# Performance work log

Measured on AMD Instinct MI355X. Metric: run time of the kernel, lower is better.

Reference implementation:

```python
import jax, jax.numpy as jnp
import numpy as np

B, S, D_IN, D_H, D_OUT = 32, 512, 512, 1024, 512


def setup_inputs() -> dict:
    key = jax.random.key(0)
    ks = jax.random.split(key, 12)
    sc_g = 1.0 / np.sqrt(D_IN + D_H)
    sc_fc = 1.0 / np.sqrt(D_H)
    return {
        "x": jax.random.normal(ks[0], (B, S, D_IN), jnp.float32),
        "W_f": jax.random.normal(ks[1], (D_IN + D_H, D_H), jnp.float32) * sc_g,
        "b_f": jax.random.normal(ks[2], (D_H,), jnp.float32) * sc_g,
        "W_i": jax.random.normal(ks[3], (D_IN + D_H, D_H), jnp.float32) * sc_g,
        "b_i": jax.random.normal(ks[4], (D_H,), jnp.float32) * sc_g,
        "W_g": jax.random.normal(ks[5], (D_IN + D_H, D_H), jnp.float32) * sc_g,
        "b_g": jax.random.normal(ks[6], (D_H,), jnp.float32) * sc_g,
        "W_o": jax.random.normal(ks[7], (D_IN + D_H, D_H), jnp.float32) * sc_g,
        "b_o": jax.random.normal(ks[8], (D_H,), jnp.float32) * sc_g,
        "W_fc": jax.random.normal(ks[9], (D_H, D_OUT), jnp.float32) * sc_fc,
        "b_fc": jax.random.normal(ks[10], (D_OUT,), jnp.float32) * sc_fc,
    }


def _lstm(x, W_f, b_f, W_i, b_i, W_g, b_g, W_o, b_o, W_fc, b_fc):
    b, s, _ = x.shape
    h0 = jnp.zeros((b, W_f.shape[1]), x.dtype)
    c0 = jnp.zeros_like(h0)

    def step(carry, x_t):
        h, c = carry
        comb = jnp.concatenate([x_t, h], axis=1)  # [B, D_in+D_h]
        f = jax.nn.sigmoid(comb @ W_f + b_f)
        i = jax.nn.sigmoid(comb @ W_i + b_i)
        g = jnp.tanh(comb @ W_g + b_g)
        o = jax.nn.sigmoid(comb @ W_o + b_o)
        c = f * c + i * g
        h = o * jnp.tanh(c)
        return (h, c), h

    _, hs = jax.lax.scan(step, (h0, c0), jnp.swapaxes(x, 0, 1))  # [S, B, D_h]
    hs = jnp.swapaxes(hs, 0, 1)  # [B, S, D_h]
    return hs @ W_fc + b_fc  # [B, S, D_out]


def reference(x, W_f, b_f, W_i, b_i, W_g, b_g, W_o, b_o, W_fc, b_fc):
    return _lstm(x, W_f, b_f, W_i, b_i, W_g, b_g, W_o, b_o, W_fc, b_fc)
```

## Files before the change

### kernel.cpp

```cpp
#include <hip/hip_runtime.h>

typedef short short8 __attribute__((ext_vector_type(8)));
typedef float f32x4 __attribute__((ext_vector_type(4)));
typedef unsigned short u16;

#define Bz   32
#define Sz   512
#define DIN  512
#define DH   1024
#define DOUT 512
#define KTOT 1536
#define NWG  256
#define NTH  256
#define TPW  12

__device__ __forceinline__ u16 bf_rne(float f) {
  unsigned b = __float_as_uint(f);
  return (u16)((b + 0x7fffu + ((b >> 16) & 1u)) >> 16);
}
__device__ __forceinline__ float bf_f(u16 h) { return __uint_as_float(((unsigned)h) << 16); }
__device__ __forceinline__ void bf_split(float f, u16& hi, u16& lo) {
  hi = bf_rne(f);
  lo = bf_rne(f - bf_f(hi));
}

__device__ __forceinline__ float sigm(float v) { return 1.0f / (1.0f + __expf(-v)); }

__device__ __forceinline__ f32x4 mfma16(short8 a, short8 b, f32x4 c) {
  return __builtin_amdgcn_mfma_f32_16x16x32_bf16(a, b, c, 0, 0, 0);
}

__device__ __forceinline__ void grid_bar(unsigned* __restrict__ arrive,
                                         unsigned* __restrict__ rel,
                                         int wg, int tid, unsigned round) {
  __syncthreads();
  if (wg == 0) {
    if (tid > 0) {
      while (__hip_atomic_load(&arrive[tid * 32], __ATOMIC_RELAXED,
                               __HIP_MEMORY_SCOPE_AGENT) < round)
        __builtin_amdgcn_s_sleep(1);
    }
    __builtin_amdgcn_fence(__ATOMIC_ACQUIRE, "agent");
    __syncthreads();
    if (tid == 0)
      __hip_atomic_store(rel, round, __ATOMIC_RELEASE, __HIP_MEMORY_SCOPE_AGENT);
  } else {
    if (tid == 0) {
      __hip_atomic_store(&arrive[wg * 32], round, __ATOMIC_RELEASE,
                         __HIP_MEMORY_SCOPE_AGENT);
      while (__hip_atomic_load(rel, __ATOMIC_RELAXED,
                               __HIP_MEMORY_SCOPE_AGENT) < round)
        __builtin_amdgcn_s_sleep(1);
      __builtin_amdgcn_fence(__ATOMIC_ACQUIRE, "agent");
    }
    __syncthreads();
  }
}

__global__ __launch_bounds__(256)
void xsplit(const float* __restrict__ x, u16* __restrict__ xhi, u16* __restrict__ xlo) {
  const int i = (blockIdx.x * 256 + threadIdx.x) * 4;
  const float4 v = *(const float4*)(x + i);
  u16 h0, l0, h1, l1, h2, l2, h3, l3;
  bf_split(v.x, h0, l0); bf_split(v.y, h1, l1);
  bf_split(v.z, h2, l2); bf_split(v.w, h3, l3);
  ushort4 hv = {h0, h1, h2, h3}, lv = {l0, l1, l2, l3};
  *(ushort4*)(xhi + i) = hv;
  *(ushort4*)(xlo + i) = lv;
}

__global__ __launch_bounds__(NTH, 1)
void lstm_rec(const u16* __restrict__ xhi, const u16* __restrict__ xlo,
              const float* __restrict__ Wf, const float* __restrict__ bfv,
              const float* __restrict__ Wi, const float* __restrict__ biv,
              const float* __restrict__ Wg, const float* __restrict__ bgv,
              const float* __restrict__ Wo, const float* __restrict__ bov,
              u16* __restrict__ hhi, u16* __restrict__ hlo,
              float* __restrict__ hs,
              unsigned* __restrict__ arrive, unsigned* __restrict__ rel)
{
  __shared__ __align__(16) float pdump[4][2][64][4];
  __shared__ float csh[Bz][4];
  __shared__ float bsh[16];

  const int tid  = threadIdx.x;
  const int wg   = blockIdx.x;
  const int wid  = tid >> 6;
  const int lane = tid & 63;
  const int c    = lane & 15;
  const int q    = lane >> 4;
  const int g    = c & 3;
  const int jl   = c >> 2;
  const int col  = wg * 4 + jl;

  const float* Wsrc = (g == 0) ? Wf : (g == 1) ? Wi : (g == 2) ? Wg : Wo;
  short8 Bhi[TPW], Blo[TPW];
  #pragma unroll
  for (int tt = 0; tt < TPW; ++tt) {
    const int k0 = (wid * TPW + tt) * 32 + q * 8;
    short8 bh, bl;
    #pragma unroll
    for (int i = 0; i < 8; ++i) {
      u16 h, l;
      bf_split(Wsrc[(k0 + i) * DH + col], h, l);
      bh[i] = (short)h; bl[i] = (short)l;
    }
    Bhi[tt] = bh; Blo[tt] = bl;
  }
  if (tid < 16) {
    const int g2 = tid & 3;
    const float* bsrc = (g2 == 0) ? bfv : (g2 == 1) ? biv : (g2 == 2) ? bgv : bov;
    bsh[tid] = bsrc[wg * 4 + (tid >> 2)];
  }
  if (tid < 128) {
    csh[tid & 31][tid >> 5] = 0.0f;
    const int idx = wg * 128 + tid;
    hhi[idx] = 0; hlo[idx] = 0;
  }
  grid_bar(arrive, rel, wg, tid, 1u);

  const int bA = lane & 15;

  for (int t = 0; t < Sz; ++t) {
    const u16* __restrict__ hh = hhi + (t & 1) * (Bz * DH);
    const u16* __restrict__ hl = hlo + (t & 1) * (Bz * DH);

    f32x4 a_hh0 = {0.f,0.f,0.f,0.f}, a_hl0 = a_hh0, a_lh0 = a_hh0;
    f32x4 a_hh1 = a_hh0, a_hl1 = a_hh0, a_lh1 = a_hh0;

    #pragma unroll
    for (int tt = 0; tt < TPW; ++tt) {
      const int k = (wid * TPW + tt) * 32 + q * 8;
      short8 Ah0, Al0, Ah1, Al1;
      if (k < DIN) {
        Ah0 = *(const short8*)(xhi + ((bA * Sz + t) * DIN + k));
        Ah1 = *(const short8*)(xhi + (((bA + 16) * Sz + t) * DIN + k));
        Al0 = *(const short8*)(xlo + ((bA * Sz + t) * DIN + k));
        Al1 = *(const short8*)(xlo + (((bA + 16) * Sz + t) * DIN + k));
      } else {
        const int kh = k - DIN;
        Ah0 = *(const short8*)(hh + bA * DH + kh);
        Ah1 = *(const short8*)(hh + (bA + 16) * DH + kh);
        Al0 = *(const short8*)(hl + bA * DH + kh);
        Al1 = *(const short8*)(hl + (bA + 16) * DH + kh);
      }
      a_hh0 = mfma16(Ah0, Bhi[tt], a_hh0);
      a_hl0 = mfma16(Ah0, Blo[tt], a_hl0);
      a_lh0 = mfma16(Al0, Bhi[tt], a_lh0);
      a_hh1 = mfma16(Ah1, Bhi[tt], a_hh1);
      a_hl1 = mfma16(Ah1, Blo[tt], a_hl1);
      a_lh1 = mfma16(Al1, Bhi[tt], a_lh1);
    }
    const f32x4 acc0 = a_hh0 + a_hl0 + a_lh0;
    const f32x4 acc1 = a_hh1 + a_hl1 + a_lh1;
    *(f32x4*)&pdump[wid][0][lane][0] = acc0;
    *(f32x4*)&pdump[wid][1][lane][0] = acc1;
    __syncthreads();

    if (tid < 128) {
      const int b = tid & 31, j = tid >> 5;
      const int m = b >> 4, r = b & 15, rg = r & 3;
      float G[4];
      #pragma unroll
      for (int g2 = 0; g2 < 4; ++g2) {
        const int ln = (r >> 2) * 16 + (j * 4 + g2);
        G[g2] = bsh[j * 4 + g2] + pdump[0][m][ln][rg] + pdump[1][m][ln][rg]
              + pdump[2][m][ln][rg] + pdump[3][m][ln][rg];
      }
      const float fv = sigm(G[0]);
      const float iv = sigm(G[1]);
      const float gv = tanhf(G[2]);
      const float ov = sigm(G[3]);
      const float cn = fv * csh[b][j] + iv * gv;
      csh[b][j] = cn;
      const float hv = ov * tanhf(cn);
      u16 hx, lx; bf_split(hv, hx, lx);
      const int par = ((t + 1) & 1) * (Bz * DH);
      hhi[par + b * DH + wg * 4 + j] = hx;
      hlo[par + b * DH + wg * 4 + j] = lx;
      hs[(b * Sz + t) * DH + wg * 4 + j] = hv;
    }
    grid_bar(arrive, rel, wg, tid, (unsigned)(t + 2));
  }
}

__global__ __launch_bounds__(256)
void lstm_fc(const float* __restrict__ hs, const float* __restrict__ Wfc,
             const float* __restrict__ bfc, float* __restrict__ out)
{
  __shared__ __align__(16) float Ash[16][68];
  __shared__ __align__(16) float Bsh[16][68];
  const int tid = threadIdx.x;
  const int mt = (int)(blockIdx.x >> 3) * 64;
  const int nt = (int)(blockIdx.x & 7) * 64;
  const int ty = tid >> 4, tx = tid & 15;
  const int am = tid & 63, ak = (tid >> 6) * 4;
  const int bk = tid >> 4, bn = (tid & 15) * 4;
  float acc[4][4] = {};
  for (int k0 = 0; k0 < DH; k0 += 16) {
    const float4 av = *(const float4*)&hs[(mt + am) * DH + k0 + ak];
    const float4 bv = *(const float4*)&Wfc[(k0 + bk) * DOUT + nt + bn];
    Ash[ak + 0][am] = av.x;
    Ash[ak + 1][am] = av.y;
    Ash[ak + 2][am] = av.z;
    Ash[ak + 3][am] = av.w;
    *(float4*)&Bsh[bk][bn] = bv;
    __syncthreads();
    #pragma unroll
    for (int kk = 0; kk < 16; ++kk) {
      const float4 a = *(const float4*)&Ash[kk][ty * 4];
      const float4 b = *(const float4*)&Bsh[kk][tx * 4];
      const float avv[4] = {a.x, a.y, a.z, a.w};
      const float bvv[4] = {b.x, b.y, b.z, b.w};
      #pragma unroll
      for (int i = 0; i < 4; ++i)
        #pragma unroll
        for (int j = 0; j < 4; ++j)
          acc[i][j] = fmaf(avv[i], bvv[j], acc[i][j]);
    }
    __syncthreads();
  }
  const float4 bb = *(const float4*)&bfc[nt + tx * 4];
  const float bias[4] = {bb.x, bb.y, bb.z, bb.w};
  #pragma unroll
  for (int i = 0; i < 4; ++i) {
    float4 o;
    o.x = acc[i][0] + bias[0];
    o.y = acc[i][1] + bias[1];
    o.z = acc[i][2] + bias[2];
    o.w = acc[i][3] + bias[3];
    *(float4*)&out[(mt + ty * 4 + i) * DOUT + nt + tx * 4] = o;
  }
}

extern "C" void kernel_launch(void* const* d_in, const int* in_sizes, int n_in,
                              void* d_out, int out_size, void* d_ws, size_t ws_size,
                              hipStream_t stream) {
  const float* x   = (const float*)d_in[0];
  const float* Wf  = (const float*)d_in[1];
  const float* bf  = (const float*)d_in[2];
  const float* Wi  = (const float*)d_in[3];
  const float* bi  = (const float*)d_in[4];
  const float* Wg  = (const float*)d_in[5];
  const float* bg  = (const float*)d_in[6];
  const float* Wo  = (const float*)d_in[7];
  const float* bo  = (const float*)d_in[8];
  const float* Wfc = (const float*)d_in[9];
  const float* bfc = (const float*)d_in[10];
  float* out = (float*)d_out;

  char* w = (char*)d_ws;
  unsigned* arrive = (unsigned*)w;
  unsigned* rel    = (unsigned*)(w + 32768);
  size_t off = 65536;
  u16* hhi = (u16*)(w + off);                         off += 2u * Bz * DH * sizeof(u16);
  u16* hlo = (u16*)(w + off);                         off += 2u * Bz * DH * sizeof(u16);
  u16* xhi = (u16*)(w + off);                         off += (size_t)Bz * Sz * DIN * sizeof(u16);
  u16* xlo = (u16*)(w + off);                         off += (size_t)Bz * Sz * DIN * sizeof(u16);
  float* hs = (float*)(w + off);

  hipMemsetAsync(d_ws, 0, 65536, stream);

  const int xN = Bz * Sz * DIN;
  hipLaunchKernelGGL(xsplit, dim3(xN / (256 * 4)), dim3(256), 0, stream, x, xhi, xlo);

  hipLaunchKernelGGL(lstm_rec, dim3(NWG), dim3(NTH), 0, stream,
                     xhi, xlo, Wf, bf, Wi, bi, Wg, bg, Wo, bo, hhi, hlo, hs,
                     arrive, rel);

  hipLaunchKernelGGL(lstm_fc, dim3((Bz * Sz / 64) * (DOUT / 64)), dim3(256), 0, stream,
                     hs, Wfc, bfc, out);
}
```

Measured before the change: 11.09 ms.

## Halve recurrent workgroups and replace master-release grid barrier with all-to-all polling

The recurrent kernel now runs 128 workgroups of 512 threads, each computing 8 hidden columns with two column sub-groups of four waves, instead of 256 workgroups of 4 columns. The grid barrier drops the central release flag: every workgroup publishes its arrival and then polls all arrival flags directly. The aim is to cut the per-timestep barrier latency by removing the extra master-to-worker round trip and halving the number of participants. The cost is more polling traffic on the flag cache lines and larger workgroups holding weight fragments in registers.

```diff
diff --git a/kernel.cpp b/kernel.cpp
--- a/kernel.cpp
+++ b/kernel.cpp
@@ -10,8 +10,8 @@
 #define DH   1024
 #define DOUT 512
 #define KTOT 1536
-#define NWG  256
-#define NTH  256
+#define NWG  128
+#define NTH  512
 #define TPW  12
 
 __device__ __forceinline__ u16 bf_rne(float f) {
@@ -31,30 +31,18 @@
 }
 
 __device__ __forceinline__ void grid_bar(unsigned* __restrict__ arrive,
-                                         unsigned* __restrict__ rel,
                                          int wg, int tid, unsigned round) {
   __syncthreads();
-  if (wg == 0) {
-    if (tid > 0) {
-      while (__hip_atomic_load(&arrive[tid * 32], __ATOMIC_RELAXED,
-                               __HIP_MEMORY_SCOPE_AGENT) < round)
-        __builtin_amdgcn_s_sleep(1);
-    }
-    __builtin_amdgcn_fence(__ATOMIC_ACQUIRE, "agent");
-    __syncthreads();
-    if (tid == 0)
-      __hip_atomic_store(rel, round, __ATOMIC_RELEASE, __HIP_MEMORY_SCOPE_AGENT);
-  } else {
-    if (tid == 0) {
-      __hip_atomic_store(&arrive[wg * 32], round, __ATOMIC_RELEASE,
-                         __HIP_MEMORY_SCOPE_AGENT);
-      while (__hip_atomic_load(rel, __ATOMIC_RELAXED,
-                               __HIP_MEMORY_SCOPE_AGENT) < round)
-        __builtin_amdgcn_s_sleep(1);
-      __builtin_amdgcn_fence(__ATOMIC_ACQUIRE, "agent");
-    }
-    __syncthreads();
-  }
+  if (tid == 0)
+    __hip_atomic_store(&arrive[wg * 32], round, __ATOMIC_RELEASE,
+                       __HIP_MEMORY_SCOPE_AGENT);
+  if (tid < NWG) {
+    while (__hip_atomic_load(&arrive[tid * 32], __ATOMIC_RELAXED,
+                             __HIP_MEMORY_SCOPE_AGENT) < round)
+      __builtin_amdgcn_s_sleep(2);
+  }
+  __builtin_amdgcn_fence(__ATOMIC_ACQUIRE, "agent");
+  __syncthreads();
 }
 
 __global__ __launch_bounds__(256)
@@ -77,27 +65,29 @@
               const float* __restrict__ Wo, const float* __restrict__ bov,
               u16* __restrict__ hhi, u16* __restrict__ hlo,
               float* __restrict__ hs,
-              unsigned* __restrict__ arrive, unsigned* __restrict__ rel)
+              unsigned* __restrict__ arrive)
 {
-  __shared__ __align__(16) float pdump[4][2][64][4];
-  __shared__ float csh[Bz][4];
-  __shared__ float bsh[16];
+  __shared__ __align__(16) float pdump[8][2][64][4];
+  __shared__ float csh[Bz][8];
+  __shared__ float bsh[32];
 
   const int tid  = threadIdx.x;
   const int wg   = blockIdx.x;
   const int wid  = tid >> 6;
   const int lane = tid & 63;
+  const int kwid = wid & 3;
+  const int nsub = wid >> 2;
   const int c    = lane & 15;
   const int q    = lane >> 4;
   const int g    = c & 3;
   const int jl   = c >> 2;
-  const int col  = wg * 4 + jl;
+  const int col  = wg * 8 + nsub * 4 + jl;
 
   const float* Wsrc = (g == 0) ? Wf : (g == 1) ? Wi : (g == 2) ? Wg : Wo;
   short8 Bhi[TPW], Blo[TPW];
   #pragma unroll
   for (int tt = 0; tt < TPW; ++tt) {
-    const int k0 = (wid * TPW + tt) * 32 + q * 8;
+    const int k0 = (kwid * TPW + tt) * 32 + q * 8;
     short8 bh, bl;
     #pragma unroll
     for (int i = 0; i < 8; ++i) {
@@ -107,17 +97,17 @@
     }
     Bhi[tt] = bh; Blo[tt] = bl;
   }
-  if (tid < 16) {
+  if (tid < 32) {
     const int g2 = tid & 3;
     const float* bsrc = (g2 == 0) ? bfv : (g2 == 1) ? biv : (g2 == 2) ? bgv : bov;
-    bsh[tid] = bsrc[wg * 4 + (tid >> 2)];
-  }
-  if (tid < 128) {
+    bsh[tid] = bsrc[wg * 8 + (tid >> 2)];
+  }
+  if (tid < 256) {
     csh[tid & 31][tid >> 5] = 0.0f;
-    const int idx = wg * 128 + tid;
+    const int idx = wg * 256 + tid;
     hhi[idx] = 0; hlo[idx] = 0;
   }
-  grid_bar(arrive, rel, wg, tid, 1u);
+  grid_bar(arrive, wg, tid, 1u);
 
   const int bA = lane & 15;
 
@@ -130,7 +120,7 @@
 
     #pragma unroll
     for (int tt = 0; tt < TPW; ++tt) {
-      const int k = (wid * TPW + tt) * 32 + q * 8;
+      const int k = (kwid * TPW + tt) * 32 + q * 8;
       short8 Ah0, Al0, Ah1, Al1;
       if (k < DIN) {
         Ah0 = *(const short8*)(xhi + ((bA * Sz + t) * DIN + k));
@@ -157,30 +147,32 @@
     *(f32x4*)&pdump[wid][1][lane][0] = acc1;
     __syncthreads();
 
-    if (tid < 128) {
-      const int b = tid & 31, j = tid >> 5;
+    if (tid < 256) {
+      const int b = tid & 31, jj = tid >> 5;
       const int m = b >> 4, r = b & 15, rg = r & 3;
+      const int ns = jj >> 2, ji = jj & 3;
       float G[4];
       #pragma unroll
       for (int g2 = 0; g2 < 4; ++g2) {
-        const int ln = (r >> 2) * 16 + (j * 4 + g2);
-        G[g2] = bsh[j * 4 + g2] + pdump[0][m][ln][rg] + pdump[1][m][ln][rg]
-              + pdump[2][m][ln][rg] + pdump[3][m][ln][rg];
+        const int ln = (r >> 2) * 16 + (ji * 4 + g2);
+        G[g2] = bsh[jj * 4 + g2]
+              + pdump[ns * 4 + 0][m][ln][rg] + pdump[ns * 4 + 1][m][ln][rg]
+              + pdump[ns * 4 + 2][m][ln][rg] + pdump[ns * 4 + 3][m][ln][rg];
       }
       const float fv = sigm(G[0]);
       const float iv = sigm(G[1]);
       const float gv = tanhf(G[2]);
       const float ov = sigm(G[3]);
-      const float cn = fv * csh[b][j] + iv * gv;
-      csh[b][j] = cn;
+      const float cn = fv * csh[b][jj] + iv * gv;
+      csh[b][jj] = cn;
       const float hv = ov * tanhf(cn);
       u16 hx, lx; bf_split(hv, hx, lx);
       const int par = ((t + 1) & 1) * (Bz * DH);
-      hhi[par + b * DH + wg * 4 + j] = hx;
-      hlo[par + b * DH + wg * 4 + j] = lx;
-      hs[(b * Sz + t) * DH + wg * 4 + j] = hv;
-    }
-    grid_bar(arrive, rel, wg, tid, (unsigned)(t + 2));
+      hhi[par + b * DH + wg * 8 + jj] = hx;
+      hlo[par + b * DH + wg * 8 + jj] = lx;
+      hs[(b * Sz + t) * DH + wg * 8 + jj] = hv;
+    }
+    grid_bar(arrive, wg, tid, (unsigned)(t + 2));
   }
 }
 
@@ -251,7 +243,6 @@
 
   char* w = (char*)d_ws;
   unsigned* arrive = (unsigned*)w;
-  unsigned* rel    = (unsigned*)(w + 32768);
   size_t off = 65536;
   u16* hhi = (u16*)(w + off);                         off += 2u * Bz * DH * sizeof(u16);
   u16* hlo = (u16*)(w + off);                         off += 2u * Bz * DH * sizeof(u16);
@@ -266,7 +257,7 @@
 
   hipLaunchKernelGGL(lstm_rec, dim3(NWG), dim3(NTH), 0, stream,
                      xhi, xlo, Wf, bf, Wi, bi, Wg, bg, Wo, bo, hhi, hlo, hs,
-                     arrive, rel);
+                     arrive);
 
   hipLaunchKernelGGL(lstm_fc, dim3((Bz * Sz / 64) * (DOUT / 64)), dim3(256), 0, stream,
                      hs, Wfc, bfc, out);
```

New measurement: 12.88 ms. +16.1%, slower.
